# Optimization experiments

Measured on AMD Instinct MI355X. Metric: run time of the kernel, lower is better.

The kernel has to match this reference:

```python
import jax, jax.numpy as jnp
import numpy as np

B, N, C, OUT, E = 8, 16384, 128, 256, 262144


def setup_inputs() -> dict:
    key = jax.random.key(0)
    k1, k2, k3 = jax.random.split(key, 3)
    x = jax.random.normal(k1, (B, N, C), dtype=jnp.float32)
    edge_index = jax.random.randint(k2, (2, E), 0, N, dtype=jnp.int64)
    W = jax.random.normal(k3, (C, OUT), dtype=jnp.float32) * 0.02
    b = jnp.zeros((OUT,), dtype=jnp.float32)
    return {"x": x, "edge_index": edge_index, "W": W, "b": b}


def reference(x, edge_index, W, b):
    # x: (B, N, C); edge_index: (2, E) shared across the batch (as in the torch code,
    # which repeats row/col B times with batch offsets -> equivalent to per-batch segment max).
    row, col = edge_index[0], edge_index[1]
    n = x.shape[1]

    def agg_one(xb):  # xb: (N, C)
        x_j = xb[col]  # gather neighbor features, (E, C)
        a = jax.ops.segment_max(x_j, row, num_segments=n)  # amax scatter-reduce
        # nodes with no incoming edge: torch fills -1e9 then zeros them; segment_max gives -inf
        return jnp.where(jnp.isfinite(a), a, 0.0)

    aggr = jax.vmap(agg_one)(x) - x  # max-relative: max_j(x_j) - x_i, (B, N, C)
    h = jnp.einsum("bnc,co->bno", aggr, W) + b
    return jax.nn.gelu(h, approximate=False)  # torch nn.GELU() is exact erf GELU
```

## Files before the change

kernel.cpp:

```cpp
#include <hip/hip_runtime.h>
#include <hip/hip_bf16.h>

#define B_   8
#define N_   16384
#define C_   128
#define OUT_ 256
#define E_   262144

#define CNT_OFF  0u
#define OVFC_OFF 16384u
#define OVF_OFF  16448u
#define TAB_OFF  540736u
#define WT_OFF   1589312u
#define XBF_OFF  1605696u
#define AGGR_OFF 9994304u

typedef __attribute__((ext_vector_type(8))) short bf16x8;
typedef __attribute__((ext_vector_type(4))) float f32x4;

__device__ __forceinline__ unsigned short f2bf(float f) {
  unsigned u = __float_as_uint(f);
  u += 0x7FFFu + ((u >> 16) & 1u);
  return (unsigned short)(u >> 16);
}
__device__ __forceinline__ float gelu_exact(float v) {
  return 0.5f * v * (1.0f + erff(v * 0.70710678118654752f));
}
__device__ __forceinline__ unsigned umin_(unsigned a, unsigned b) {
  return a < b ? a : b;
}

__global__ __launch_bounds__(256) void k_prep(const float* __restrict__ x,
                                              const unsigned* __restrict__ eidx,
                                              const float* __restrict__ W,
                                              unsigned* __restrict__ ws) {
  const unsigned bid = blockIdx.x, tid = threadIdx.x;
  if (bid < 16384u) {
    unsigned i = bid * 256u + tid;
    float4 v = ((const float4*)x)[i];
    uint2 o;
    o.x = (unsigned)f2bf(v.x) | ((unsigned)f2bf(v.y) << 16);
    o.y = (unsigned)f2bf(v.z) | ((unsigned)f2bf(v.w) << 16);
    ((uint2*)(ws + XBF_OFF))[i] = o;
  } else if (bid < 17408u) {
    __shared__ int flag32;
    if (tid == 0) flag32 = 0;
    __syncthreads();
    unsigned e = (bid - 16384u) * 256u + tid;
    if (eidx[2u * e + 1u] != 0u) flag32 = 1;
    __syncthreads();
    int row, col;
    if (flag32) {
      row = (int)eidx[e];
      col = (int)eidx[e + E_];
    } else {
      const long long* p = (const long long*)eidx;
      row = (int)p[e];
      col = (int)p[e + E_];
    }
    unsigned pos = atomicAdd(ws + CNT_OFF + (unsigned)row, 1u);
    if (pos < 64u) {
      ws[TAB_OFF + ((unsigned)row << 6) + pos] = (unsigned)col;
    } else {
      unsigned o = atomicAdd(ws + OVFC_OFF, 1u);
      ws[OVF_OFF + 2u * o]      = (unsigned)row;
      ws[OVF_OFF + 2u * o + 1u] = (unsigned)col;
    }
  } else {
    unsigned t = (bid - 17408u) * 256u + tid;
    unsigned n = t >> 7, k = t & 127u;
    ((unsigned short*)(ws + WT_OFF))[n * 128u + k] = f2bf(W[k * 256u + n]);
  }
}

__global__ __launch_bounds__(256) void k_aggr(const uint4* __restrict__ xbf4,
                                              const unsigned* __restrict__ ws,
                                              uint4* __restrict__ aggr4) {
  const unsigned bi = blockIdx.x;
  const unsigned b  = bi & 7u;
  const unsigned rg = bi >> 3;
  const unsigned row = (rg << 2) | (threadIdx.x >> 6);
  const unsigned lane = threadIdx.x & 63u;
  const unsigned g  = lane >> 4;
  const unsigned ln = lane & 15u;
  const uint4* xb = xbf4 + ((size_t)b << 18);

  const unsigned deg = ws[CNT_OFF + row];
  const bool has = (deg != 0u);
  const unsigned d64 = deg < 64u ? deg : 64u;

  const unsigned cpre = ws[TAB_OFF + (row << 6) + lane];
  const uint4 xw = xb[((size_t)row << 4) + ln];

  float mlo[4], mhi[4];
#pragma unroll
  for (int r = 0; r < 4; ++r) { mlo[r] = -INFINITY; mhi[r] = -INFINITY; }

#define MAX1(a, r)                                                          \
  mhi[r] = fmaxf(mhi[r], __uint_as_float(a));                               \
  mlo[r] = fmaxf(mlo[r], __uint_as_float((a) << 16));
#define MAX2(a, c, r)                                                       \
  mhi[r] = fmaxf(mhi[r], fmaxf(__uint_as_float(a), __uint_as_float(c)));    \
  mlo[r] = fmaxf(mlo[r],                                                    \
      fmaxf(__uint_as_float((a) << 16), __uint_as_float((c) << 16)));

  if (has) {
    const unsigned dm1 = d64 - 1u;
    if (d64 <= 16u) {
      unsigned c0 = (unsigned)__shfl((int)cpre, (int)umin_(g,       dm1));
      unsigned c1 = (unsigned)__shfl((int)cpre, (int)umin_(4u + g,  dm1));
      unsigned c2 = (unsigned)__shfl((int)cpre, (int)umin_(8u + g,  dm1));
      unsigned c3 = (unsigned)__shfl((int)cpre, (int)umin_(12u + g, dm1));
      uint4 u0 = xb[((size_t)c0 << 4) + ln];
      uint4 u1 = xb[((size_t)c1 << 4) + ln];
      uint4 u2 = xb[((size_t)c2 << 4) + ln];
      uint4 u3 = xb[((size_t)c3 << 4) + ln];
      MAX2(u0.x, u1.x, 0) MAX2(u0.y, u1.y, 1)
      MAX2(u0.z, u1.z, 2) MAX2(u0.w, u1.w, 3)
      MAX2(u2.x, u3.x, 0) MAX2(u2.y, u3.y, 1)
      MAX2(u2.z, u3.z, 2) MAX2(u2.w, u3.w, 3)
    } else if (d64 <= 32u) {
      unsigned c[8];
#pragma unroll
      for (int i = 0; i < 8; ++i)
        c[i] = (unsigned)__shfl((int)cpre, (int)umin_(4u * i + g, dm1));
      uint4 u[8];
#pragma unroll
      for (int i = 0; i < 8; ++i) u[i] = xb[((size_t)c[i] << 4) + ln];
#pragma unroll
      for (int i = 0; i < 8; i += 2) {
        MAX2(u[i].x, u[i + 1].x, 0) MAX2(u[i].y, u[i + 1].y, 1)
        MAX2(u[i].z, u[i + 1].z, 2) MAX2(u[i].w, u[i + 1].w, 3)
      }
    } else {
      for (unsigned t = 0u; t < d64; t += 16u) {
        unsigned c0 = (unsigned)__shfl((int)cpre, (int)umin_(t + g,       dm1));
        unsigned c1 = (unsigned)__shfl((int)cpre, (int)umin_(t + 4u + g,  dm1));
        unsigned c2 = (unsigned)__shfl((int)cpre, (int)umin_(t + 8u + g,  dm1));
        unsigned c3 = (unsigned)__shfl((int)cpre, (int)umin_(t + 12u + g, dm1));
        uint4 u0 = xb[((size_t)c0 << 4) + ln];
        uint4 u1 = xb[((size_t)c1 << 4) + ln];
        uint4 u2 = xb[((size_t)c2 << 4) + ln];
        uint4 u3 = xb[((size_t)c3 << 4) + ln];
        MAX2(u0.x, u1.x, 0) MAX2(u0.y, u1.y, 1)
        MAX2(u0.z, u1.z, 2) MAX2(u0.w, u1.w, 3)
        MAX2(u2.x, u3.x, 0) MAX2(u2.y, u3.y, 1)
        MAX2(u2.z, u3.z, 2) MAX2(u2.w, u3.w, 3)
      }
    }
  }
  if (deg > 64u) {
    unsigned no = ws[OVFC_OFF];
    for (unsigned i = 0u; i < no; i += 4u) {
      unsigned k = i + g;
      if (k < no && ws[OVF_OFF + 2u * k] == row) {
        unsigned c = ws[OVF_OFF + 2u * k + 1u];
        uint4 u = xb[((size_t)c << 4) + ln];
        MAX1(u.x, 0) MAX1(u.y, 1) MAX1(u.z, 2) MAX1(u.w, 3)
      }
    }
  }
#undef MAX1
#undef MAX2

#pragma unroll
  for (int r = 0; r < 4; ++r) {
    mlo[r] = fmaxf(mlo[r], __shfl_xor(mlo[r], 16, 64));
    mhi[r] = fmaxf(mhi[r], __shfl_xor(mhi[r], 16, 64));
  }
#pragma unroll
  for (int r = 0; r < 4; ++r) {
    mlo[r] = fmaxf(mlo[r], __shfl_xor(mlo[r], 32, 64));
    mhi[r] = fmaxf(mhi[r], __shfl_xor(mhi[r], 32, 64));
  }

  if (g == 0u) {
    unsigned xv[4] = {xw.x, xw.y, xw.z, xw.w};
    unsigned ox[4];
#pragma unroll
    for (int r = 0; r < 4; ++r) {
      float vlo = has ? mlo[r] : 0.0f;
      float vhi = has ? __uint_as_float(__float_as_uint(mhi[r]) & 0xFFFF0000u)
                      : 0.0f;
      unsigned lo = f2bf(vlo - __uint_as_float(xv[r] << 16));
      unsigned hi = f2bf(vhi - __uint_as_float(xv[r] & 0xFFFF0000u));
      ox[r] = lo | (hi << 16);
    }
    uint4 o = {ox[0], ox[1], ox[2], ox[3]};
    aggr4[(((size_t)b << 14) + row) * 16u + ln] = o;
  }
}

__global__ __launch_bounds__(256, 4) void k_gemm(const unsigned short* __restrict__ aggr,
                                                 const unsigned short* __restrict__ Wt,
                                                 const float* __restrict__ bias,
                                                 float* __restrict__ out) {
  __shared__ unsigned short Wt_sm[128 * 136];
  const int tid = threadIdx.x;
  const int mbase = blockIdx.x * 64;

  const int lane = tid & 63;
  const int wv = tid >> 6;
  const int ln = lane & 15;
  const int q = lane >> 4;

  const unsigned short* arow = aggr + (size_t)(mbase + wv * 16 + ln) * 128 + q * 8;
  bf16x8 af[4];
#pragma unroll
  for (int kc = 0; kc < 4; ++kc) af[kc] = *(const bf16x8*)(arow + kc * 32);

#pragma unroll
  for (int half = 0; half < 2; ++half) {
    const int nbase = half * 128;
#pragma unroll
    for (int i = 0; i < 8; ++i) {
      int slot = i * 256 + tid;
      int n = slot >> 4, k8 = slot & 15;
      uint4 u = *(const uint4*)(Wt + (size_t)(nbase + n) * 128 + k8 * 8);
      *(uint4*)&Wt_sm[n * 136 + k8 * 8] = u;
    }
    __syncthreads();

    f32x4 acc[8];
#pragma unroll
    for (int f = 0; f < 8; ++f) acc[f] = (f32x4){0.f, 0.f, 0.f, 0.f};

#pragma unroll
    for (int kc = 0; kc < 4; ++kc) {
#pragma unroll
      for (int f = 0; f < 8; ++f) {
        bf16x8 bf = *(const bf16x8*)&Wt_sm[(f * 16 + ln) * 136 + kc * 32 + q * 8];
        acc[f] = __builtin_amdgcn_mfma_f32_16x16x32_bf16(af[kc], bf, acc[f], 0, 0, 0);
      }
    }

#pragma unroll
    for (int f = 0; f < 8; ++f) {
      int n = nbase + f * 16 + ln;
      float bv = bias[n];
#pragma unroll
      for (int r = 0; r < 4; ++r) {
        int m = mbase + wv * 16 + q * 4 + r;
        out[(size_t)m * 256 + n] = gelu_exact(acc[f][r] + bv);
      }
    }
    __syncthreads();
  }
}

extern "C" void kernel_launch(void* const* d_in, const int* in_sizes, int n_in,
                              void* d_out, int out_size, void* d_ws, size_t ws_size,
                              hipStream_t stream) {
  const float* x      = (const float*)d_in[0];
  const unsigned* eid = (const unsigned*)d_in[1];
  const float* W      = (const float*)d_in[2];
  const float* bia    = (const float*)d_in[3];
  float* out          = (float*)d_out;
  unsigned* ws        = (unsigned*)d_ws;

  unsigned short* Wt   = (unsigned short*)(ws + WT_OFF);
  unsigned short* aggr = (unsigned short*)(ws + AGGR_OFF);

  hipMemsetAsync(ws + CNT_OFF, 0, 16448 * sizeof(unsigned), stream);
  hipLaunchKernelGGL(k_prep, dim3(17536), dim3(256), 0, stream, x, eid, W, ws);
  hipLaunchKernelGGL(k_aggr, dim3(32768), dim3(256), 0, stream,
                     (const uint4*)(ws + XBF_OFF), ws, (uint4*)(ws + AGGR_OFF));
  hipLaunchKernelGGL(k_gemm, dim3(2048),  dim3(256), 0, stream,
                     aggr, Wt, bia, out);
}
```

Measured before the change: 289.4 us.

## Fuse max-relative aggregation into GEMM kernel via shared-memory staging

Merges the aggregation kernel and the GEMM+GELU kernel into one. Each block aggregates 64 rows (each wave handles 16 rows, two at a time) into LDS as bf16, then runs the MFMA GEMM from that LDS tile. This removes the global write and re-read of the aggregated tensor and one kernel launch. The cost is less parallelism during the gather phase: far fewer waves are in flight, each doing a serial loop over 8 row pairs, which may hide gather latency worse than the old 32768-block launch.

```diff
diff --git a/kernel.cpp b/kernel.cpp
--- a/kernel.cpp
+++ b/kernel.cpp
@@ -13,7 +13,6 @@
 #define TAB_OFF  540736u
 #define WT_OFF   1589312u
 #define XBF_OFF  1605696u
-#define AGGR_OFF 9994304u
 
 typedef __attribute__((ext_vector_type(8))) short bf16x8;
 typedef __attribute__((ext_vector_type(4))) float f32x4;
@@ -73,175 +72,167 @@
   }
 }
 
-__global__ __launch_bounds__(256) void k_aggr(const uint4* __restrict__ xbf4,
-                                              const unsigned* __restrict__ ws,
-                                              uint4* __restrict__ aggr4) {
+__global__ __launch_bounds__(256, 4) void k_ag(const uint4* __restrict__ xbf4,
+                                               const unsigned* __restrict__ ws,
+                                               const unsigned short* __restrict__ Wt,
+                                               const float* __restrict__ bias,
+                                               float* __restrict__ out) {
+  __shared__ unsigned short sm[128 * 136];
   const unsigned bi = blockIdx.x;
   const unsigned b  = bi & 7u;
-  const unsigned rg = bi >> 3;
-  const unsigned row = (rg << 2) | (threadIdx.x >> 6);
-  const unsigned lane = threadIdx.x & 63u;
+  const unsigned mbase = (bi >> 3) << 6;
+  const unsigned tid = threadIdx.x;
+  const unsigned wv = tid >> 6;
+  const unsigned lane = tid & 63u;
   const unsigned g  = lane >> 4;
   const unsigned ln = lane & 15u;
   const uint4* xb = xbf4 + ((size_t)b << 18);
-
-  const unsigned deg = ws[CNT_OFF + row];
-  const bool has = (deg != 0u);
-  const unsigned d64 = deg < 64u ? deg : 64u;
-
-  const unsigned cpre = ws[TAB_OFF + (row << 6) + lane];
-  const uint4 xw = xb[((size_t)row << 4) + ln];
-
-  float mlo[4], mhi[4];
-#pragma unroll
-  for (int r = 0; r < 4; ++r) { mlo[r] = -INFINITY; mhi[r] = -INFINITY; }
-
-#define MAX1(a, r)                                                          \
-  mhi[r] = fmaxf(mhi[r], __uint_as_float(a));                               \
-  mlo[r] = fmaxf(mlo[r], __uint_as_float((a) << 16));
-#define MAX2(a, c, r)                                                       \
-  mhi[r] = fmaxf(mhi[r], fmaxf(__uint_as_float(a), __uint_as_float(c)));    \
-  mlo[r] = fmaxf(mlo[r],                                                    \
-      fmaxf(__uint_as_float((a) << 16), __uint_as_float((c) << 16)));
-
-  if (has) {
-    const unsigned dm1 = d64 - 1u;
-    if (d64 <= 16u) {
-      unsigned c0 = (unsigned)__shfl((int)cpre, (int)umin_(g,       dm1));
-      unsigned c1 = (unsigned)__shfl((int)cpre, (int)umin_(4u + g,  dm1));
-      unsigned c2 = (unsigned)__shfl((int)cpre, (int)umin_(8u + g,  dm1));
-      unsigned c3 = (unsigned)__shfl((int)cpre, (int)umin_(12u + g, dm1));
-      uint4 u0 = xb[((size_t)c0 << 4) + ln];
-      uint4 u1 = xb[((size_t)c1 << 4) + ln];
-      uint4 u2 = xb[((size_t)c2 << 4) + ln];
-      uint4 u3 = xb[((size_t)c3 << 4) + ln];
-      MAX2(u0.x, u1.x, 0) MAX2(u0.y, u1.y, 1)
-      MAX2(u0.z, u1.z, 2) MAX2(u0.w, u1.w, 3)
-      MAX2(u2.x, u3.x, 0) MAX2(u2.y, u3.y, 1)
-      MAX2(u2.z, u3.z, 2) MAX2(u2.w, u3.w, 3)
-    } else if (d64 <= 32u) {
-      unsigned c[8];
-#pragma unroll
-      for (int i = 0; i < 8; ++i)
-        c[i] = (unsigned)__shfl((int)cpre, (int)umin_(4u * i + g, dm1));
-      uint4 u[8];
-#pragma unroll
-      for (int i = 0; i < 8; ++i) u[i] = xb[((size_t)c[i] << 4) + ln];
-#pragma unroll
-      for (int i = 0; i < 8; i += 2) {
-        MAX2(u[i].x, u[i + 1].x, 0) MAX2(u[i].y, u[i + 1].y, 1)
-        MAX2(u[i].z, u[i + 1].z, 2) MAX2(u[i].w, u[i + 1].w, 3)
-      }
-    } else {
-      for (unsigned t = 0u; t < d64; t += 16u) {
-        unsigned c0 = (unsigned)__shfl((int)cpre, (int)umin_(t + g,       dm1));
-        unsigned c1 = (unsigned)__shfl((int)cpre, (int)umin_(t + 4u + g,  dm1));
-        unsigned c2 = (unsigned)__shfl((int)cpre, (int)umin_(t + 8u + g,  dm1));
-        unsigned c3 = (unsigned)__shfl((int)cpre, (int)umin_(t + 12u + g, dm1));
-        uint4 u0 = xb[((size_t)c0 << 4) + ln];
-        uint4 u1 = xb[((size_t)c1 << 4) + ln];
-        uint4 u2 = xb[((size_t)c2 << 4) + ln];
-        uint4 u3 = xb[((size_t)c3 << 4) + ln];
-        MAX2(u0.x, u1.x, 0) MAX2(u0.y, u1.y, 1)
-        MAX2(u0.z, u1.z, 2) MAX2(u0.w, u1.w, 3)
-        MAX2(u2.x, u3.x, 0) MAX2(u2.y, u3.y, 1)
-        MAX2(u2.z, u3.z, 2) MAX2(u2.w, u3.w, 3)
-      }
+  const unsigned wbase = mbase + (wv << 4);
+
+#define MAXU4(U, ml, mh)                                                    \
+  mh[0] = fmaxf(mh[0], __uint_as_float((U).x));                             \
+  ml[0] = fmaxf(ml[0], __uint_as_float((U).x << 16));                       \
+  mh[1] = fmaxf(mh[1], __uint_as_float((U).y));                             \
+  ml[1] = fmaxf(ml[1], __uint_as_float((U).y << 16));                       \
+  mh[2] = fmaxf(mh[2], __uint_as_float((U).z));                             \
+  ml[2] = fmaxf(ml[2], __uint_as_float((U).z << 16));                       \
+  mh[3] = fmaxf(mh[3], __uint_as_float((U).w));                             \
+  ml[3] = fmaxf(ml[3], __uint_as_float((U).w << 16));
+
+  for (unsigned i = 0u; i < 16u; i += 2u) {
+    const unsigned ra = wbase + i, rb = ra + 1u;
+    const unsigned dega = ws[CNT_OFF + ra];
+    const unsigned degb = ws[CNT_OFF + rb];
+    const unsigned d64a = dega < 64u ? dega : 64u;
+    const unsigned d64b = degb < 64u ? degb : 64u;
+    const unsigned dm1a = d64a - 1u;
+    const unsigned dm1b = d64b - 1u;
+    const unsigned tva = ws[TAB_OFF + (ra << 6) + lane];
+    const unsigned tvb = ws[TAB_OFF + (rb << 6) + lane];
+    const unsigned cprea = dega ? tva : ra;
+    const unsigned cpreb = degb ? tvb : rb;
+    const uint4 xwa = xb[((size_t)ra << 4) + ln];
+    const uint4 xwb = xb[((size_t)rb << 4) + ln];
+
+    float mloa[4], mhia[4], mlob[4], mhib[4];
+#pragma unroll
+    for (int r = 0; r < 4; ++r) {
+      mloa[r] = -INFINITY; mhia[r] = -INFINITY;
+      mlob[r] = -INFINITY; mhib[r] = -INFINITY;
+    }
+
+    if (dega | degb) {
+      const unsigned mx = d64a > d64b ? d64a : d64b;
+      for (unsigned t = 0u; t < mx; t += 16u) {
+        unsigned ca[4], cb[4];
+#pragma unroll
+        for (int k = 0; k < 4; ++k) {
+          unsigned e = t + 4u * (unsigned)k + g;
+          ca[k] = (unsigned)__shfl((int)cprea, (int)umin_(umin_(e, dm1a), 63u));
+          cb[k] = (unsigned)__shfl((int)cpreb, (int)umin_(umin_(e, dm1b), 63u));
+        }
+        uint4 ua[4], ub[4];
+#pragma unroll
+        for (int k = 0; k < 4; ++k) ua[k] = xb[((size_t)ca[k] << 4) + ln];
+#pragma unroll
+        for (int k = 0; k < 4; ++k) ub[k] = xb[((size_t)cb[k] << 4) + ln];
+#pragma unroll
+        for (int k = 0; k < 4; ++k) { MAXU4(ua[k], mloa, mhia) }
+#pragma unroll
+        for (int k = 0; k < 4; ++k) { MAXU4(ub[k], mlob, mhib) }
+      }
+    }
+    if ((dega > 64u) | (degb > 64u)) {
+      unsigned no = ws[OVFC_OFF];
+      for (unsigned k2 = g; k2 < no; k2 += 4u) {
+        unsigned rr = ws[OVF_OFF + 2u * k2];
+        if (rr == ra) {
+          uint4 u = xb[((size_t)ws[OVF_OFF + 2u * k2 + 1u] << 4) + ln];
+          MAXU4(u, mloa, mhia)
+        } else if (rr == rb) {
+          uint4 u = xb[((size_t)ws[OVF_OFF + 2u * k2 + 1u] << 4) + ln];
+          MAXU4(u, mlob, mhib)
+        }
+      }
+    }
+
+#pragma unroll
+    for (int r = 0; r < 4; ++r) {
+      mloa[r] = fmaxf(mloa[r], __shfl_xor(mloa[r], 16, 64));
+      mhia[r] = fmaxf(mhia[r], __shfl_xor(mhia[r], 16, 64));
+      mloa[r] = fmaxf(mloa[r], __shfl_xor(mloa[r], 32, 64));
+      mhia[r] = fmaxf(mhia[r], __shfl_xor(mhia[r], 32, 64));
+      mlob[r] = fmaxf(mlob[r], __shfl_xor(mlob[r], 16, 64));
+      mhib[r] = fmaxf(mhib[r], __shfl_xor(mhib[r], 16, 64));
+      mlob[r] = fmaxf(mlob[r], __shfl_xor(mlob[r], 32, 64));
+      mhib[r] = fmaxf(mhib[r], __shfl_xor(mhib[r], 32, 64));
+    }
+
+    if (g == 0u) {
+      const bool hasa = (dega != 0u), hasb = (degb != 0u);
+      unsigned xva[4] = {xwa.x, xwa.y, xwa.z, xwa.w};
+      unsigned xvb[4] = {xwb.x, xwb.y, xwb.z, xwb.w};
+      unsigned oxa[4], oxb[4];
+#pragma unroll
+      for (int r = 0; r < 4; ++r) {
+        float vloa = hasa ? mloa[r] : 0.0f;
+        float vhia = hasa ? __uint_as_float(__float_as_uint(mhia[r]) & 0xFFFF0000u) : 0.0f;
+        oxa[r] = (unsigned)f2bf(vloa - __uint_as_float(xva[r] << 16)) |
+                 ((unsigned)f2bf(vhia - __uint_as_float(xva[r] & 0xFFFF0000u)) << 16);
+        float vlob = hasb ? mlob[r] : 0.0f;
+        float vhib = hasb ? __uint_as_float(__float_as_uint(mhib[r]) & 0xFFFF0000u) : 0.0f;
+        oxb[r] = (unsigned)f2bf(vlob - __uint_as_float(xvb[r] << 16)) |
+                 ((unsigned)f2bf(vhib - __uint_as_float(xvb[r] & 0xFFFF0000u)) << 16);
+      }
+      uint4 oa = {oxa[0], oxa[1], oxa[2], oxa[3]};
+      uint4 ob = {oxb[0], oxb[1], oxb[2], oxb[3]};
+      *(uint4*)&sm[wv * 2176u + i * 136u + ln * 8u]        = oa;
+      *(uint4*)&sm[wv * 2176u + (i + 1u) * 136u + ln * 8u] = ob;
     }
   }
-  if (deg > 64u) {
-    unsigned no = ws[OVFC_OFF];
-    for (unsigned i = 0u; i < no; i += 4u) {
-      unsigned k = i + g;
-      if (k < no && ws[OVF_OFF + 2u * k] == row) {
-        unsigned c = ws[OVF_OFF + 2u * k + 1u];
-        uint4 u = xb[((size_t)c << 4) + ln];
-        MAX1(u.x, 0) MAX1(u.y, 1) MAX1(u.z, 2) MAX1(u.w, 3)
-      }
-    }
-  }
-#undef MAX1
-#undef MAX2
-
-#pragma unroll
-  for (int r = 0; r < 4; ++r) {
-    mlo[r] = fmaxf(mlo[r], __shfl_xor(mlo[r], 16, 64));
-    mhi[r] = fmaxf(mhi[r], __shfl_xor(mhi[r], 16, 64));
-  }
-#pragma unroll
-  for (int r = 0; r < 4; ++r) {
-    mlo[r] = fmaxf(mlo[r], __shfl_xor(mlo[r], 32, 64));
-    mhi[r] = fmaxf(mhi[r], __shfl_xor(mhi[r], 32, 64));
-  }
-
-  if (g == 0u) {
-    unsigned xv[4] = {xw.x, xw.y, xw.z, xw.w};
-    unsigned ox[4];
-#pragma unroll
-    for (int r = 0; r < 4; ++r) {
-      float vlo = has ? mlo[r] : 0.0f;
-      float vhi = has ? __uint_as_float(__float_as_uint(mhi[r]) & 0xFFFF0000u)
-                      : 0.0f;
-      unsigned lo = f2bf(vlo - __uint_as_float(xv[r] << 16));
-      unsigned hi = f2bf(vhi - __uint_as_float(xv[r] & 0xFFFF0000u));
-      ox[r] = lo | (hi << 16);
-    }
-    uint4 o = {ox[0], ox[1], ox[2], ox[3]};
-    aggr4[(((size_t)b << 14) + row) * 16u + ln] = o;
-  }
-}
-
-__global__ __launch_bounds__(256, 4) void k_gemm(const unsigned short* __restrict__ aggr,
-                                                 const unsigned short* __restrict__ Wt,
-                                                 const float* __restrict__ bias,
-                                                 float* __restrict__ out) {
-  __shared__ unsigned short Wt_sm[128 * 136];
-  const int tid = threadIdx.x;
-  const int mbase = blockIdx.x * 64;
-
-  const int lane = tid & 63;
-  const int wv = tid >> 6;
-  const int ln = lane & 15;
-  const int q = lane >> 4;
-
-  const unsigned short* arow = aggr + (size_t)(mbase + wv * 16 + ln) * 128 + q * 8;
+#undef MAXU4
+
+  __syncthreads();
+
+  const unsigned q = g;
   bf16x8 af[4];
 #pragma unroll
-  for (int kc = 0; kc < 4; ++kc) af[kc] = *(const bf16x8*)(arow + kc * 32);
+  for (int kc = 0; kc < 4; ++kc)
+    af[kc] = *(const bf16x8*)&sm[wv * 2176u + ln * 136u + (unsigned)kc * 32u + q * 8u];
+  __syncthreads();
 
 #pragma unroll
   for (int half = 0; half < 2; ++half) {
     const int nbase = half * 128;
 #pragma unroll
     for (int i = 0; i < 8; ++i) {
-      int slot = i * 256 + tid;
+      int slot = i * 256 + (int)tid;
       int n = slot >> 4, k8 = slot & 15;
       uint4 u = *(const uint4*)(Wt + (size_t)(nbase + n) * 128 + k8 * 8);
-      *(uint4*)&Wt_sm[n * 136 + k8 * 8] = u;
+      *(uint4*)&sm[n * 136 + k8 * 8] = u;
     }
     __syncthreads();
 
     f32x4 acc[8];
 #pragma unroll
     for (int f = 0; f < 8; ++f) acc[f] = (f32x4){0.f, 0.f, 0.f, 0.f};
-
 #pragma unroll
     for (int kc = 0; kc < 4; ++kc) {
 #pragma unroll
       for (int f = 0; f < 8; ++f) {
-        bf16x8 bf = *(const bf16x8*)&Wt_sm[(f * 16 + ln) * 136 + kc * 32 + q * 8];
+        bf16x8 bf = *(const bf16x8*)&sm[(f * 16 + (int)ln) * 136 + kc * 32 + (int)q * 8];
         acc[f] = __builtin_amdgcn_mfma_f32_16x16x32_bf16(af[kc], bf, acc[f], 0, 0, 0);
       }
     }
 
 #pragma unroll
     for (int f = 0; f < 8; ++f) {
-      int n = nbase + f * 16 + ln;
+      int n = nbase + f * 16 + (int)ln;
       float bv = bias[n];
 #pragma unroll
       for (int r = 0; r < 4; ++r) {
-        int m = mbase + wv * 16 + q * 4 + r;
-        out[(size_t)m * 256 + n] = gelu_exact(acc[f][r] + bv);
+        unsigned mrow = ((size_t)b << 14) + mbase + (wv << 4) + q * 4u + (unsigned)r;
+        out[(size_t)mrow * 256 + n] = gelu_exact(acc[f][r] + bv);
       }
     }
     __syncthreads();
@@ -258,13 +249,10 @@
   float* out          = (float*)d_out;
   unsigned* ws        = (unsigned*)d_ws;
 
-  unsigned short* Wt   = (unsigned short*)(ws + WT_OFF);
-  unsigned short* aggr = (unsigned short*)(ws + AGGR_OFF);
+  const unsigned short* Wt = (const unsigned short*)(ws + WT_OFF);
 
   hipMemsetAsync(ws + CNT_OFF, 0, 16448 * sizeof(unsigned), stream);
   hipLaunchKernelGGL(k_prep, dim3(17536), dim3(256), 0, stream, x, eid, W, ws);
-  hipLaunchKernelGGL(k_aggr, dim3(32768), dim3(256), 0, stream,
-                     (const uint4*)(ws + XBF_OFF), ws, (uint4*)(ws + AGGR_OFF));
-  hipLaunchKernelGGL(k_gemm, dim3(2048),  dim3(256), 0, stream,
-                     aggr, Wt, bia, out);
-}
+  hipLaunchKernelGGL(k_ag,   dim3(2048),  dim3(256), 0, stream,
+                     (const uint4*)(ws + XBF_OFF), ws, Wt, bia, out);
+}
```

Measured after the change: 284.6 us. About the same (-1.7%).
